# Kernel tuning notes

Measured on AMD Instinct MI355X. Metric: run time of the kernel, lower is better.

Reference implementation:

```python
import jax, jax.numpy as jnp
import numpy as np
from jax import lax

B, Hm, Wm = 8, 128, 128          # batch, mesh height, mesh width
DIM, HEADS, DH, G, K = 128, 8, 64, 64, 3
INNER = HEADS * DH
N = Hm * Wm


def setup_inputs() -> dict:
    key = jax.random.key(0)
    ks = jax.random.split(key, 12)
    s = 0.02
    x = jax.random.normal(ks[0], (B, N, DIM), dtype=jnp.float32)
    conv_fx_w = jax.random.normal(ks[1], (K, K, DIM, INNER), dtype=jnp.float32) * s
    conv_fx_b = jnp.zeros((INNER,), dtype=jnp.float32)
    conv_x_w = jax.random.normal(ks[2], (K, K, DIM, INNER), dtype=jnp.float32) * s
    conv_x_b = jnp.zeros((INNER,), dtype=jnp.float32)
    # nn.Linear(dim_head, slice_num): weight (G, DH), orthogonal-init approximated by scaled normal
    slice_w = jax.random.normal(ks[3], (G, DH), dtype=jnp.float32) * (1.0 / np.sqrt(DH))
    slice_b = jnp.zeros((G,), dtype=jnp.float32)
    temperature = jnp.ones((1, HEADS, 1, 1), dtype=jnp.float32) * 0.5
    wq = jax.random.normal(ks[4], (DH, DH), dtype=jnp.float32) * s
    wk = jax.random.normal(ks[5], (DH, DH), dtype=jnp.float32) * s
    wv = jax.random.normal(ks[6], (DH, DH), dtype=jnp.float32) * s
    out_w = jax.random.normal(ks[7], (DIM, INNER), dtype=jnp.float32) * s
    out_b = jnp.zeros((DIM,), dtype=jnp.float32)
    return {
        "x": x,
        "conv_fx_w": conv_fx_w, "conv_fx_b": conv_fx_b,
        "conv_x_w": conv_x_w, "conv_x_b": conv_x_b,
        "slice_w": slice_w, "slice_b": slice_b,
        "temperature": temperature,
        "wq": wq, "wk": wk, "wv": wv,
        "out_w": out_w, "out_b": out_b,
    }


def _conv(z, w, b):
    # z: (B, H, W, Cin); w: (K, K, Cin, Cout); SAME padding, stride 1
    return lax.conv_general_dilated(
        z, w, window_strides=(1, 1), padding="SAME",
        dimension_numbers=("NHWC", "HWIO", "NHWC")) + b


def reference(x, conv_fx_w, conv_fx_b, conv_x_w, conv_x_b,
              slice_w, slice_b, temperature, wq, wk, wv, out_w, out_b):
    b, n, c = x.shape
    xi = x.reshape(b, Hm, Wm, c)
    # (B,H,W,INNER) -> (B,N,heads,dh) -> (B,heads,N,dh)
    fx_mid = _conv(xi, conv_fx_w, conv_fx_b).reshape(b, n, HEADS, DH).transpose(0, 2, 1, 3)
    x_mid = _conv(xi, conv_x_w, conv_x_b).reshape(b, n, HEADS, DH).transpose(0, 2, 1, 3)

    temp = jnp.clip(temperature, 0.1, 5.0)  # (1,heads,1,1)
    logits = (jnp.einsum("bhnc,gc->bhng", x_mid, slice_w) + slice_b) / temp
    slice_weights = jax.nn.softmax(logits, axis=-1)         # (B,heads,N,G)

    slice_norm = slice_weights.sum(axis=2)                   # (B,heads,G)
    slice_token = jnp.einsum("bhnc,bhng->bhgc", fx_mid, slice_weights)
    slice_token = slice_token / (slice_norm + 1e-5)[..., None]

    q = jnp.einsum("bhgc,dc->bhgd", slice_token, wq)
    k = jnp.einsum("bhgc,dc->bhgd", slice_token, wk)
    v = jnp.einsum("bhgc,dc->bhgd", slice_token, wv)

    scale = DH ** (-0.5)
    attn = jax.nn.softmax(jnp.einsum("bhgd,bhkd->bhgk", q, k) * scale, axis=-1)
    out_slice = jnp.einsum("bhgk,bhkd->bhgd", attn, v)       # (B,heads,G,dh)

    out_x = jnp.einsum("bhgc,bhng->bhnc", out_slice, slice_weights)
    out_x = out_x.transpose(0, 2, 1, 3).reshape(b, n, INNER)
    return jnp.einsum("bnc,dc->bnd", out_x, out_w) + out_b
```

## Files before the change

### kernel.cpp

```cpp
#include <hip/hip_runtime.h>
#include <stdint.h>

#define BATCH 8
#define HEADS 8
#define HM 128
#define WM 128
#define NPIX (HM*WM)
#define DIMC 128
#define DH 64
#define GS 64
#define INNER 512
#define KTOT 1152
#define XT_LD 128
#define PT_LD 128

typedef unsigned short u16;
typedef short v8s __attribute__((ext_vector_type(8)));
typedef float v4f __attribute__((ext_vector_type(4)));

__device__ __forceinline__ u16 f2bf(float f) {
    unsigned x = __float_as_uint(f);
    return (u16)((x + 0x7fffu + ((x >> 16) & 1u)) >> 16);
}
__device__ __forceinline__ float bf2f(u16 u) { return __uint_as_float(((unsigned)u) << 16); }
__device__ __forceinline__ unsigned cvtpk(float lo, float hi) {
    unsigned r;
    asm("v_cvt_pk_bf16_f32 %0, %1, %2" : "=v"(r) : "v"(lo), "v"(hi));
    return r;
}

union BF8 { uint4 v; u16 s[8]; };

__global__ __launch_bounds__(256) void k_build_w(
    const float* __restrict__ wx, const float* __restrict__ wfx,
    const float* __restrict__ slw, const float* __restrict__ temp,
    u16* __restrict__ wcatT, u16* __restrict__ wfxT)
{
    __shared__ float sw_l[GS][DH + 1];
    __shared__ float wx_l[INNER];
    int row = blockIdx.x;
    int t = threadIdx.x;
    for (int i = t; i < GS * DH; i += 256) sw_l[i >> 6][i & 63] = slw[i];
    for (int i = t; i < INNER; i += 256) wx_l[i] = wx[(size_t)row * INNER + i];
    __syncthreads();
#pragma unroll
    for (int j = 0; j < 2; j++) {
        int co = j * 256 + t;
        int h = co >> 6, g = co & 63;
        float s = 0.f;
        for (int c = 0; c < DH; c++) s = fmaf(wx_l[h * 64 + c], sw_l[g][c], s);
        float tv = fminf(fmaxf(temp[h], 0.1f), 5.0f);
        wcatT[(size_t)co * KTOT + row] = f2bf(s / tv);
        wfxT[(size_t)co * KTOT + row] = f2bf(wfx[(size_t)row * INNER + co]);
    }
}

__global__ __launch_bounds__(512) void k_build_b(
    const float* __restrict__ bx, const float* __restrict__ slw,
    const float* __restrict__ slb, const float* __restrict__ temp,
    float* __restrict__ bcatL)
{
    int co = threadIdx.x;
    int h = co >> 6, g = co & 63;
    float s = slb[g];
    for (int c = 0; c < DH; c++) s = fmaf(bx[h * 64 + c], slw[g * 64 + c], s);
    float tv = fminf(fmaxf(temp[h], 0.1f), 5.0f);
    bcatL[co] = s / tv;
}

union SmemC {
    u16 X[130 * XT_LD];
    struct { u16 SwT[128][PT_LD]; u16 FxT[128][PT_LD]; } e;
};

__global__ __launch_bounds__(512) void k_conv2(
    const float* __restrict__ xin, const u16* __restrict__ wcatT,
    const u16* __restrict__ wfxT, const float* __restrict__ bcatL,
    const float* __restrict__ bfx, u16* __restrict__ swbT,
    float* __restrict__ straw, float* __restrict__ norm)
{
    __shared__ SmemC sm;
    int pt = blockIdx.x;
    int b = pt >> 7, y = pt & 127;
    int ct = blockIdx.y;
    int cob = ct << 8;
    int t = threadIdx.x;
    int lane = t & 63, wave = t >> 6;
    int w_half = wave >> 2, w_co = wave & 3;
    int l16 = lane & 15, lk = lane >> 4;
    int hb = b * HEADS + 4 * ct;

    v4f accL[4][4], accF[4][4];
#pragma unroll
    for (int i = 0; i < 4; i++)
#pragma unroll
        for (int j = 0; j < 4; j++) {
            accL[i][j] = v4f{0.f, 0.f, 0.f, 0.f};
            accF[i][j] = v4f{0.f, 0.f, 0.f, 0.f};
        }

    const u16* wlb[4]; const u16* wfb[4];
#pragma unroll
    for (int nj = 0; nj < 4; nj++) {
        size_t roff = (size_t)(cob + w_co * 64 + nj * 16 + l16) * KTOT + lk * 8;
        wlb[nj] = wcatT + roff;
        wfb[nj] = wfxT + roff;
    }

    v8s bL[2][4], bF[2][4];
#pragma unroll
    for (int nj = 0; nj < 4; nj++) {
        bL[0][nj] = *(const v8s*)(wlb[nj]);
        bF[0][nj] = *(const v8s*)(wfb[nj]);
    }

#pragma unroll
    for (int ky = 0; ky < 3; ky++) {
        int yy = y + ky - 1;
        bool yok = (unsigned)yy < (unsigned)HM;
        const float* xrow = xin + ((size_t)b * NPIX + (size_t)yy * WM) * DIMC;
        if (ky) __syncthreads();
#pragma unroll
        for (int it = 0; it < 5; it++) {
            int i = t + it * 512;
            if (i < 2080) {
                int row = i >> 4, k8 = i & 15;
                int px = row - 1;
                uint4 o;
                if (yok && (unsigned)px < (unsigned)WM) {
                    const float4* p = (const float4*)(xrow + (size_t)px * DIMC + k8 * 8);
                    float4 fa = p[0], fb = p[1];
                    o = make_uint4(cvtpk(fa.x, fa.y), cvtpk(fa.z, fa.w),
                                   cvtpk(fb.x, fb.y), cvtpk(fb.z, fb.w));
                } else {
                    o = make_uint4(0u, 0u, 0u, 0u);
                }
                *(uint4*)(sm.X + row * XT_LD + ((k8 ^ (row & 7)) * 8)) = o;
            }
        }
        __syncthreads();
#pragma unroll
        for (int cc = 0; cc < 12; cc++) {
            int g = ky * 12 + cc;
            if (g < 35) {
                int wo = ((g + 1) >> 2) * 128 + ((g + 1) & 3) * 32;
#pragma unroll
                for (int nj = 0; nj < 4; nj++) {
                    bL[(cc + 1) & 1][nj] = *(const v8s*)(wlb[nj] + wo);
                    bF[(cc + 1) & 1][nj] = *(const v8s*)(wfb[nj] + wo);
                }
            }
            int kx = cc >> 2, c4 = cc & 3;
            int xr7 = (l16 + kx) & 7;
            const u16* xb = sm.X + (w_half * 64 + l16 + kx) * XT_LD;
            int xo = (((c4 * 4 + lk) ^ xr7) * 8);
            v8s av[4];
#pragma unroll
            for (int mi = 0; mi < 4; mi++)
                av[mi] = *(const v8s*)(xb + mi * 16 * XT_LD + xo);
#pragma unroll
            for (int mi = 0; mi < 4; mi++)
#pragma unroll
                for (int nj = 0; nj < 4; nj++) {
                    accL[mi][nj] = __builtin_amdgcn_mfma_f32_16x16x32_bf16(
                        av[mi], bL[cc & 1][nj], accL[mi][nj], 0, 0, 0);
                    accF[mi][nj] = __builtin_amdgcn_mfma_f32_16x16x32_bf16(
                        av[mi], bF[cc & 1][nj], accF[mi][nj], 0, 0, 0);
                }
        }
    }
    __syncthreads();

    float bbL[4], bbF[4];
#pragma unroll
    for (int nj = 0; nj < 4; nj++) {
        bbL[nj] = bcatL[cob + w_co * 64 + nj * 16 + l16];
        bbF[nj] = bfx[cob + w_co * 64 + nj * 16 + l16];
    }

#pragma unroll
    for (int mi = 0; mi < 4; mi++) {
#pragma unroll
        for (int q = 0; q < 4; q++) {
            float m = accL[mi][0][q] + bbL[0];
#pragma unroll
            for (int nj = 1; nj < 4; nj++) m = fmaxf(m, accL[mi][nj][q] + bbL[nj]);
            m = fmaxf(m, __shfl_xor(m, 1));
            m = fmaxf(m, __shfl_xor(m, 2));
            m = fmaxf(m, __shfl_xor(m, 4));
            m = fmaxf(m, __shfl_xor(m, 8));
            float ssum = 0.f;
#pragma unroll
            for (int nj = 0; nj < 4; nj++) {
                float e = __expf(accL[mi][nj][q] + bbL[nj] - m);
                accL[mi][nj][q] = e; ssum += e;
            }
            ssum += __shfl_xor(ssum, 1);
            ssum += __shfl_xor(ssum, 2);
            ssum += __shfl_xor(ssum, 4);
            ssum += __shfl_xor(ssum, 8);
            float inv = 1.f / ssum;
#pragma unroll
            for (int nj = 0; nj < 4; nj++) accL[mi][nj][q] *= inv;
        }
    }

#pragma unroll
    for (int nj = 0; nj < 4; nj++) {
        float pn = 0.f;
#pragma unroll
        for (int mi = 0; mi < 4; mi++)
#pragma unroll
            for (int q = 0; q < 4; q++) pn += accL[mi][nj][q];
        pn += __shfl_xor(pn, 16);
        pn += __shfl_xor(pn, 32);
        if (lk == 0)
            atomicAdd(&norm[(size_t)(hb + w_co) * GS + nj * 16 + l16], pn);
    }

#pragma unroll
    for (int hp = 0; hp < 2; hp++) {
        bool mine = ((w_co >> 1) == hp);
        if (mine) {
            int wcp = w_co & 1;
#pragma unroll
            for (int nj = 0; nj < 4; nj++) {
                int grow = wcp * 64 + nj * 16 + l16;
                int r7 = l16 & 7;
#pragma unroll
                for (int mi = 0; mi < 4; mi++) {
                    int off = (((w_half * 8 + mi * 2 + (lk >> 1)) ^ r7) * 8) + (lk & 1) * 4;
                    uint2 wv;
                    wv.x = cvtpk(accL[mi][nj][0], accL[mi][nj][1]);
                    wv.y = cvtpk(accL[mi][nj][2], accL[mi][nj][3]);
                    *(uint2*)&sm.e.SwT[grow][off] = wv;
                    uint2 fv;
                    fv.x = cvtpk(accF[mi][nj][0] + bbF[nj], accF[mi][nj][1] + bbF[nj]);
                    fv.y = cvtpk(accF[mi][nj][2] + bbF[nj], accF[mi][nj][3] + bbF[nj]);
                    *(uint2*)&sm.e.FxT[grow][off] = fv;
                }
            }
        }
        __syncthreads();
        if (mine) {
            int wcp = w_co & 1;
            v4f pacc[2][4];
#pragma unroll
            for (int i = 0; i < 2; i++)
#pragma unroll
                for (int j = 0; j < 4; j++) pacc[i][j] = v4f{0.f, 0.f, 0.f, 0.f};
            int r7 = l16 & 7;
#pragma unroll
            for (int c = 0; c < 4; c++) {
                int ko = (((c * 4 + lk) ^ r7) * 8);
                v8s aw[2], bw[4];
#pragma unroll
                for (int mi = 0; mi < 2; mi++)
                    aw[mi] = *(const v8s*)(&sm.e.SwT[wcp * 64 + w_half * 32 + mi * 16 + l16][0] + ko);
#pragma unroll
                for (int nj = 0; nj < 4; nj++)
                    bw[nj] = *(const v8s*)(&sm.e.FxT[wcp * 64 + nj * 16 + l16][0] + ko);
#pragma unroll
                for (int mi = 0; mi < 2; mi++)
#pragma unroll
                    for (int nj = 0; nj < 4; nj++)
                        pacc[mi][nj] = __builtin_amdgcn_mfma_f32_16x16x32_bf16(
                            aw[mi], bw[nj], pacc[mi][nj], 0, 0, 0);
            }
            int bh2 = hb + 2 * hp + wcp;
#pragma unroll
            for (int mi = 0; mi < 2; mi++)
#pragma unroll
                for (int nj = 0; nj < 4; nj++)
#pragma unroll
                    for (int q = 0; q < 4; q++) {
                        int g = w_half * 32 + mi * 16 + lk * 4 + q;
                        int dh = nj * 16 + l16;
                        atomicAdd(&straw[((size_t)bh2 * GS + g) * DH + dh], pacc[mi][nj][q]);
                    }
        }
#pragma unroll
        for (int it = 0; it < 4; it++) {
            int chunk = it * 512 + t;
            int gi = chunk >> 4;
            int p8 = chunk & 15;
            uint4 v = *(const uint4*)(&sm.e.SwT[gi][0] + ((p8 ^ (gi & 7)) * 8));
            size_t di = (((size_t)(hb + 2 * hp + (gi >> 6)) * GS + (gi & 63)) * NPIX)
                        + (size_t)y * WM + p8 * 8;
            *(uint4*)&swbT[di] = v;
        }
        __syncthreads();
    }
}

__global__ __launch_bounds__(256) void k_attn(
    const float* __restrict__ straw, const float* __restrict__ norm,
    const float* __restrict__ wq, const float* __restrict__ wk, const float* __restrict__ wv,
    const float* __restrict__ outw, float* __restrict__ m1)
{
    __shared__ float lds[4][64][64];
    int bh = blockIdx.x, h = bh & 7;
    int t = threadIdx.x;
    for (int i = t; i < 4096; i += 256) {
        int g = i >> 6;
        lds[0][g][i & 63] = straw[(size_t)bh * 4096 + i] / (norm[bh * 64 + g] + 1e-5f);
    }
    __syncthreads();
    int g = t >> 2, d0 = (t & 3) << 4;
    for (int d = d0; d < d0 + 16; d++) {
        float sq = 0.f, sk = 0.f, sv = 0.f;
        for (int c = 0; c < 64; c++) {
            float sc = lds[0][g][c];
            sq = fmaf(sc, wq[d * 64 + c], sq);
            sk = fmaf(sc, wk[d * 64 + c], sk);
            sv = fmaf(sc, wv[d * 64 + c], sv);
        }
        lds[1][g][d] = sq; lds[2][g][d] = sk; lds[3][g][d] = sv;
    }
    __syncthreads();
    float attnrow[16];
    for (int k2 = d0, i = 0; k2 < d0 + 16; k2++, i++) {
        float s = 0.f;
        for (int d = 0; d < 64; d++) s = fmaf(lds[1][g][d], lds[2][k2][d], s);
        attnrow[i] = s * 0.125f;
    }
    __syncthreads();
    for (int i = 0; i < 16; i++) lds[0][g][d0 + i] = attnrow[i];
    __syncthreads();
    if (t < 64) {
        float mx = -1e30f;
        for (int j = 0; j < 64; j++) mx = fmaxf(mx, lds[0][t][j]);
        float s = 0.f;
        for (int j = 0; j < 64; j++) { float e = __expf(lds[0][t][j] - mx); lds[0][t][j] = e; s += e; }
        float inv = 1.f / s;
        for (int j = 0; j < 64; j++) lds[0][t][j] *= inv;
    }
    __syncthreads();
    float osrow[16];
    for (int d = d0, i = 0; d < d0 + 16; d++, i++) {
        float s = 0.f;
        for (int kx = 0; kx < 64; kx++) s = fmaf(lds[0][g][kx], lds[3][kx][d], s);
        osrow[i] = s;
    }
    __syncthreads();
    for (int i = 0; i < 16; i++) lds[2][g][d0 + i] = osrow[i];
    __syncthreads();
    int dimb = (t & 3) << 5;
    for (int dim = dimb; dim < dimb + 32; dim++) {
        float s = 0.f;
        for (int c = 0; c < 64; c++)
            s = fmaf(lds[2][g][c], outw[(size_t)dim * INNER + h * 64 + c], s);
        m1[((size_t)bh * 64 + g) * DIMC + dim] = s;
    }
}

__global__ __launch_bounds__(256) void k_final(
    const u16* __restrict__ swbT, const float* __restrict__ m1,
    const float* __restrict__ outb, float* __restrict__ out)
{
    __shared__ float As[32][68];
    __shared__ float Bs[32][128];
    int b = blockIdx.x, nt = blockIdx.y;
    int t = threadIdx.x;
    int tn = t & 15, tm = t >> 4;
    float acc[4][8];
#pragma unroll
    for (int i = 0; i < 4; i++)
#pragma unroll
        for (int j = 0; j < 8; j++) acc[i][j] = 0.f;
    int n0 = nt * 64;
    int gg = t >> 3, nq = (t & 7) * 8;
    int g2 = t >> 3, dd = (t & 7) * 16;
    for (int h = 0; h < HEADS; h++) {
        const u16* swp = swbT + (size_t)(b * HEADS + h) * GS * NPIX;
        const float* m1p = m1 + (size_t)(b * HEADS + h) * GS * DIMC;
        for (int g0 = 0; g0 < 64; g0 += 32) {
            __syncthreads();
            BF8 av8; av8.v = *(const uint4*)&swp[(size_t)(g0 + gg) * NPIX + n0 + nq];
#pragma unroll
            for (int i = 0; i < 8; i++) As[gg][nq + i] = bf2f(av8.s[i]);
            const float* bp = m1p + (size_t)(g0 + g2) * DIMC + dd;
            *(float4*)&Bs[g2][dd + 0]  = *(const float4*)(bp + 0);
            *(float4*)&Bs[g2][dd + 4]  = *(const float4*)(bp + 4);
            *(float4*)&Bs[g2][dd + 8]  = *(const float4*)(bp + 8);
            *(float4*)&Bs[g2][dd + 12] = *(const float4*)(bp + 12);
            __syncthreads();
#pragma unroll
            for (int kk = 0; kk < 32; kk++) {
                float4 a = *(const float4*)&As[kk][tm * 4];
                float4 b0 = *(const float4*)&Bs[kk][tn * 4];
                float4 b1 = *(const float4*)&Bs[kk][tn * 4 + 64];
                float av[4] = {a.x, a.y, a.z, a.w};
                float bv[8] = {b0.x, b0.y, b0.z, b0.w, b1.x, b1.y, b1.z, b1.w};
#pragma unroll
                for (int i = 0; i < 4; i++)
#pragma unroll
                    for (int j = 0; j < 8; j++)
                        acc[i][j] = fmaf(av[i], bv[j], acc[i][j]);
            }
        }
    }
    float4 bias0 = *(const float4*)&outb[tn * 4];
    float4 bias1 = *(const float4*)&outb[64 + tn * 4];
#pragma unroll
    for (int i = 0; i < 4; i++) {
        size_t n = (size_t)n0 + tm * 4 + i;
        size_t rb = ((size_t)b * NPIX + n) * DIMC;
        float4 r0, r1;
        r0.x = acc[i][0] + bias0.x; r0.y = acc[i][1] + bias0.y;
        r0.z = acc[i][2] + bias0.z; r0.w = acc[i][3] + bias0.w;
        r1.x = acc[i][4] + bias1.x; r1.y = acc[i][5] + bias1.y;
        r1.z = acc[i][6] + bias1.z; r1.w = acc[i][7] + bias1.w;
        *(float4*)&out[rb + tn * 4] = r0;
        *(float4*)&out[rb + 64 + tn * 4] = r1;
    }
}

extern "C" void kernel_launch(void* const* d_in, const int* in_sizes, int n_in,
                              void* d_out, int out_size, void* d_ws, size_t ws_size,
                              hipStream_t stream)
{
    (void)in_sizes; (void)n_in; (void)out_size;
    const float* x    = (const float*)d_in[0];
    const float* wfx  = (const float*)d_in[1];
    const float* bfx  = (const float*)d_in[2];
    const float* wx   = (const float*)d_in[3];
    const float* bx   = (const float*)d_in[4];
    const float* slw  = (const float*)d_in[5];
    const float* slb  = (const float*)d_in[6];
    const float* temp = (const float*)d_in[7];
    const float* wq   = (const float*)d_in[8];
    const float* wk   = (const float*)d_in[9];
    const float* wv   = (const float*)d_in[10];
    const float* outw = (const float*)d_in[11];
    const float* outb = (const float*)d_in[12];
    float* out = (float*)d_out;
    float* W = (float*)d_ws;

    u16*   wcatT = (u16*)W;
    u16*   wfxT  = (u16*)(W + 294912);
    float* bcatL = W + 589824;
    float* norm  = W + 590336;
    float* straw = W + 594432;
    float* m1    = W + 856576;
    u16*   swbT  = (u16*)(W + 1380864);
    const size_t need = 1380864ull * 4 + 67108864ull * 2;
    if (ws_size < need) return;

    hipMemsetAsync(norm, 0, (4096 + 262144) * sizeof(float), stream);

    k_build_w<<<dim3(1152), 256, 0, stream>>>(wx, wfx, slw, temp, wcatT, wfxT);
    k_build_b<<<dim3(1), 512, 0, stream>>>(bx, slw, slb, temp, bcatL);
    k_conv2<<<dim3(1024, 2), 512, 0, stream>>>(x, wcatT, wfxT, bcatL, bfx, swbT, straw, norm);
    k_attn<<<dim3(64), 256, 0, stream>>>(straw, norm, wq, wk, wv, outw, m1);
    k_final<<<dim3(8, 256), 256, 0, stream>>>(swbT, m1, outb, out);
}
```

Measured before the change: 1.192 ms.

## Shrink conv tiles to half-row, two heads per block, split conv paths across waves

Each conv block now handles a 64-pixel half row and 128 output channels (two heads) with 256 threads. Waves are split so that half compute the logit conv and half compute the fx conv, which halves accumulator registers per wave and allows 4 blocks per CU. The grid is swizzled so that consecutive blocks share inputs across channel tiles. The aim is higher occupancy and better latency hiding. In exchange, x loads are repeated more often across channel tiles, more blocks issue atomics into straw and norm, and the weight double-buffer prefetch is removed.

```diff
diff --git a/kernel.cpp b/kernel.cpp
--- a/kernel.cpp
+++ b/kernel.cpp
@@ -12,7 +12,6 @@
 #define INNER 512
 #define KTOT 1152
 #define XT_LD 128
-#define PT_LD 128
 
 typedef unsigned short u16;
 typedef short v8s __attribute__((ext_vector_type(8)));
@@ -69,50 +68,39 @@
 }
 
 union SmemC {
-    u16 X[130 * XT_LD];
-    struct { u16 SwT[128][PT_LD]; u16 FxT[128][PT_LD]; } e;
+    u16 X[66 * XT_LD];
+    struct { u16 SwT[64][64]; u16 FxT[64][64]; } e;
 };
 
-__global__ __launch_bounds__(512) void k_conv2(
+__global__ __launch_bounds__(256, 4) void k_conv2(
     const float* __restrict__ xin, const u16* __restrict__ wcatT,
     const u16* __restrict__ wfxT, const float* __restrict__ bcatL,
     const float* __restrict__ bfx, u16* __restrict__ swbT,
     float* __restrict__ straw, float* __restrict__ norm)
 {
     __shared__ SmemC sm;
-    int pt = blockIdx.x;
-    int b = pt >> 7, y = pt & 127;
-    int ct = blockIdx.y;
-    int cob = ct << 8;
+    int bid = blockIdx.x;
+    int swz = (bid & 7) * 1024 + (bid >> 3);
+    int b = swz >> 10;
+    int r = swz & 1023;
+    int y = r >> 3, half = (r >> 2) & 1, ct = r & 3;
+    int cob = ct << 7;
     int t = threadIdx.x;
     int lane = t & 63, wave = t >> 6;
-    int w_half = wave >> 2, w_co = wave & 3;
+    int w_conv = wave >> 1, w_co = wave & 1;
     int l16 = lane & 15, lk = lane >> 4;
-    int hb = b * HEADS + 4 * ct;
-
-    v4f accL[4][4], accF[4][4];
+
+    v4f acc[4][4];
 #pragma unroll
     for (int i = 0; i < 4; i++)
 #pragma unroll
-        for (int j = 0; j < 4; j++) {
-            accL[i][j] = v4f{0.f, 0.f, 0.f, 0.f};
-            accF[i][j] = v4f{0.f, 0.f, 0.f, 0.f};
-        }
-
-    const u16* wlb[4]; const u16* wfb[4];
-#pragma unroll
-    for (int nj = 0; nj < 4; nj++) {
-        size_t roff = (size_t)(cob + w_co * 64 + nj * 16 + l16) * KTOT + lk * 8;
-        wlb[nj] = wcatT + roff;
-        wfb[nj] = wfxT + roff;
-    }
-
-    v8s bL[2][4], bF[2][4];
-#pragma unroll
-    for (int nj = 0; nj < 4; nj++) {
-        bL[0][nj] = *(const v8s*)(wlb[nj]);
-        bF[0][nj] = *(const v8s*)(wfb[nj]);
-    }
+        for (int j = 0; j < 4; j++) acc[i][j] = v4f{0.f, 0.f, 0.f, 0.f};
+
+    const u16* wT = w_conv ? wfxT : wcatT;
+    const u16* wrb[4];
+#pragma unroll
+    for (int nj = 0; nj < 4; nj++)
+        wrb[nj] = wT + (size_t)(cob + w_co * 64 + nj * 16 + l16) * KTOT + lk * 8;
 
 #pragma unroll
     for (int ky = 0; ky < 3; ky++) {
@@ -122,10 +110,10 @@
         if (ky) __syncthreads();
 #pragma unroll
         for (int it = 0; it < 5; it++) {
-            int i = t + it * 512;
-            if (i < 2080) {
+            int i = t + it * 256;
+            if (i < 1056) {
                 int row = i >> 4, k8 = i & 15;
-                int px = row - 1;
+                int px = half * 64 + row - 1;
                 uint4 o;
                 if (yok && (unsigned)px < (unsigned)WM) {
                     const float4* p = (const float4*)(xrow + (size_t)px * DIMC + k8 * 8);
@@ -141,109 +129,101 @@
         __syncthreads();
 #pragma unroll
         for (int cc = 0; cc < 12; cc++) {
-            int g = ky * 12 + cc;
-            if (g < 35) {
-                int wo = ((g + 1) >> 2) * 128 + ((g + 1) & 3) * 32;
+            int kx = cc >> 2, c4 = cc & 3;
+            int wo = (ky * 3 + kx) * 128 + c4 * 32;
+            v8s bB[4];
+#pragma unroll
+            for (int nj = 0; nj < 4; nj++)
+                bB[nj] = *(const v8s*)(wrb[nj] + wo);
+            int xr7 = (l16 + kx) & 7;
+            const u16* xb = sm.X + (l16 + kx) * XT_LD;
+            int xo = (((c4 * 4 + lk) ^ xr7) * 8);
+            v8s av[4];
+#pragma unroll
+            for (int mi = 0; mi < 4; mi++)
+                av[mi] = *(const v8s*)(xb + mi * 16 * XT_LD + xo);
+#pragma unroll
+            for (int mi = 0; mi < 4; mi++)
+#pragma unroll
+                for (int nj = 0; nj < 4; nj++)
+                    acc[mi][nj] = __builtin_amdgcn_mfma_f32_16x16x32_bf16(
+                        av[mi], bB[nj], acc[mi][nj], 0, 0, 0);
+        }
+    }
+    __syncthreads();
+
+    float bb[4];
+#pragma unroll
+    for (int nj = 0; nj < 4; nj++)
+        bb[nj] = (w_conv ? bfx : bcatL)[cob + w_co * 64 + nj * 16 + l16];
+
+    if (w_conv == 0) {
+#pragma unroll
+        for (int mi = 0; mi < 4; mi++) {
+#pragma unroll
+            for (int q = 0; q < 4; q++) {
+                float m = acc[mi][0][q] + bb[0];
+#pragma unroll
+                for (int nj = 1; nj < 4; nj++) m = fmaxf(m, acc[mi][nj][q] + bb[nj]);
+                m = fmaxf(m, __shfl_xor(m, 1));
+                m = fmaxf(m, __shfl_xor(m, 2));
+                m = fmaxf(m, __shfl_xor(m, 4));
+                m = fmaxf(m, __shfl_xor(m, 8));
+                float ssum = 0.f;
 #pragma unroll
                 for (int nj = 0; nj < 4; nj++) {
-                    bL[(cc + 1) & 1][nj] = *(const v8s*)(wlb[nj] + wo);
-                    bF[(cc + 1) & 1][nj] = *(const v8s*)(wfb[nj] + wo);
+                    float e = __expf(acc[mi][nj][q] + bb[nj] - m);
+                    acc[mi][nj][q] = e; ssum += e;
+                }
+                ssum += __shfl_xor(ssum, 1);
+                ssum += __shfl_xor(ssum, 2);
+                ssum += __shfl_xor(ssum, 4);
+                ssum += __shfl_xor(ssum, 8);
+                float inv = 1.f / ssum;
+#pragma unroll
+                for (int nj = 0; nj < 4; nj++) acc[mi][nj][q] *= inv;
+            }
+        }
+#pragma unroll
+        for (int nj = 0; nj < 4; nj++) {
+            float pn = 0.f;
+#pragma unroll
+            for (int mi = 0; mi < 4; mi++)
+#pragma unroll
+                for (int q = 0; q < 4; q++) pn += acc[mi][nj][q];
+            pn += __shfl_xor(pn, 16);
+            pn += __shfl_xor(pn, 32);
+            if (lk == 0)
+                atomicAdd(&norm[(size_t)(b * HEADS + 2 * ct + w_co) * GS + nj * 16 + l16], pn);
+        }
+    }
+
+#pragma unroll
+    for (int hp = 0; hp < 2; hp++) {
+        bool mine = (w_co == hp);
+        if (mine) {
+#pragma unroll
+            for (int nj = 0; nj < 4; nj++) {
+                int grow = nj * 16 + l16;
+                int r7 = l16 & 7;
+#pragma unroll
+                for (int mi = 0; mi < 4; mi++) {
+                    int off = (((mi * 2 + (lk >> 1)) ^ r7) * 8) + (lk & 1) * 4;
+                    uint2 wv;
+                    if (w_conv == 0) {
+                        wv.x = cvtpk(acc[mi][nj][0], acc[mi][nj][1]);
+                        wv.y = cvtpk(acc[mi][nj][2], acc[mi][nj][3]);
+                        *(uint2*)&sm.e.SwT[grow][off] = wv;
+                    } else {
+                        wv.x = cvtpk(acc[mi][nj][0] + bb[nj], acc[mi][nj][1] + bb[nj]);
+                        wv.y = cvtpk(acc[mi][nj][2] + bb[nj], acc[mi][nj][3] + bb[nj]);
+                        *(uint2*)&sm.e.FxT[grow][off] = wv;
+                    }
                 }
             }
-            int kx = cc >> 2, c4 = cc & 3;
-            int xr7 = (l16 + kx) & 7;
-            const u16* xb = sm.X + (w_half * 64 + l16 + kx) * XT_LD;
-            int xo = (((c4 * 4 + lk) ^ xr7) * 8);
-            v8s av[4];
-#pragma unroll
-            for (int mi = 0; mi < 4; mi++)
-                av[mi] = *(const v8s*)(xb + mi * 16 * XT_LD + xo);
-#pragma unroll
-            for (int mi = 0; mi < 4; mi++)
-#pragma unroll
-                for (int nj = 0; nj < 4; nj++) {
-                    accL[mi][nj] = __builtin_amdgcn_mfma_f32_16x16x32_bf16(
-                        av[mi], bL[cc & 1][nj], accL[mi][nj], 0, 0, 0);
-                    accF[mi][nj] = __builtin_amdgcn_mfma_f32_16x16x32_bf16(
-                        av[mi], bF[cc & 1][nj], accF[mi][nj], 0, 0, 0);
-                }
-        }
-    }
-    __syncthreads();
-
-    float bbL[4], bbF[4];
-#pragma unroll
-    for (int nj = 0; nj < 4; nj++) {
-        bbL[nj] = bcatL[cob + w_co * 64 + nj * 16 + l16];
-        bbF[nj] = bfx[cob + w_co * 64 + nj * 16 + l16];
-    }
-
-#pragma unroll
-    for (int mi = 0; mi < 4; mi++) {
-#pragma unroll
-        for (int q = 0; q < 4; q++) {
-            float m = accL[mi][0][q] + bbL[0];
-#pragma unroll
-            for (int nj = 1; nj < 4; nj++) m = fmaxf(m, accL[mi][nj][q] + bbL[nj]);
-            m = fmaxf(m, __shfl_xor(m, 1));
-            m = fmaxf(m, __shfl_xor(m, 2));
-            m = fmaxf(m, __shfl_xor(m, 4));
-            m = fmaxf(m, __shfl_xor(m, 8));
-            float ssum = 0.f;
-#pragma unroll
-            for (int nj = 0; nj < 4; nj++) {
-                float e = __expf(accL[mi][nj][q] + bbL[nj] - m);
-                accL[mi][nj][q] = e; ssum += e;
-            }
-            ssum += __shfl_xor(ssum, 1);
-            ssum += __shfl_xor(ssum, 2);
-            ssum += __shfl_xor(ssum, 4);
-            ssum += __shfl_xor(ssum, 8);
-            float inv = 1.f / ssum;
-#pragma unroll
-            for (int nj = 0; nj < 4; nj++) accL[mi][nj][q] *= inv;
-        }
-    }
-
-#pragma unroll
-    for (int nj = 0; nj < 4; nj++) {
-        float pn = 0.f;
-#pragma unroll
-        for (int mi = 0; mi < 4; mi++)
-#pragma unroll
-            for (int q = 0; q < 4; q++) pn += accL[mi][nj][q];
-        pn += __shfl_xor(pn, 16);
-        pn += __shfl_xor(pn, 32);
-        if (lk == 0)
-            atomicAdd(&norm[(size_t)(hb + w_co) * GS + nj * 16 + l16], pn);
-    }
-
-#pragma unroll
-    for (int hp = 0; hp < 2; hp++) {
-        bool mine = ((w_co >> 1) == hp);
-        if (mine) {
-            int wcp = w_co & 1;
-#pragma unroll
-            for (int nj = 0; nj < 4; nj++) {
-                int grow = wcp * 64 + nj * 16 + l16;
-                int r7 = l16 & 7;
-#pragma unroll
-                for (int mi = 0; mi < 4; mi++) {
-                    int off = (((w_half * 8 + mi * 2 + (lk >> 1)) ^ r7) * 8) + (lk & 1) * 4;
-                    uint2 wv;
-                    wv.x = cvtpk(accL[mi][nj][0], accL[mi][nj][1]);
-                    wv.y = cvtpk(accL[mi][nj][2], accL[mi][nj][3]);
-                    *(uint2*)&sm.e.SwT[grow][off] = wv;
-                    uint2 fv;
-                    fv.x = cvtpk(accF[mi][nj][0] + bbF[nj], accF[mi][nj][1] + bbF[nj]);
-                    fv.y = cvtpk(accF[mi][nj][2] + bbF[nj], accF[mi][nj][3] + bbF[nj]);
-                    *(uint2*)&sm.e.FxT[grow][off] = fv;
-                }
-            }
         }
         __syncthreads();
         if (mine) {
-            int wcp = w_co & 1;
             v4f pacc[2][4];
 #pragma unroll
             for (int i = 0; i < 2; i++)
@@ -251,15 +231,15 @@
                 for (int j = 0; j < 4; j++) pacc[i][j] = v4f{0.f, 0.f, 0.f, 0.f};
             int r7 = l16 & 7;
 #pragma unroll
-            for (int c = 0; c < 4; c++) {
+            for (int c = 0; c < 2; c++) {
                 int ko = (((c * 4 + lk) ^ r7) * 8);
                 v8s aw[2], bw[4];
 #pragma unroll
                 for (int mi = 0; mi < 2; mi++)
-                    aw[mi] = *(const v8s*)(&sm.e.SwT[wcp * 64 + w_half * 32 + mi * 16 + l16][0] + ko);
+                    aw[mi] = *(const v8s*)(&sm.e.SwT[w_conv * 32 + mi * 16 + l16][0] + ko);
 #pragma unroll
                 for (int nj = 0; nj < 4; nj++)
-                    bw[nj] = *(const v8s*)(&sm.e.FxT[wcp * 64 + nj * 16 + l16][0] + ko);
+                    bw[nj] = *(const v8s*)(&sm.e.FxT[nj * 16 + l16][0] + ko);
 #pragma unroll
                 for (int mi = 0; mi < 2; mi++)
 #pragma unroll
@@ -267,26 +247,26 @@
                         pacc[mi][nj] = __builtin_amdgcn_mfma_f32_16x16x32_bf16(
                             aw[mi], bw[nj], pacc[mi][nj], 0, 0, 0);
             }
-            int bh2 = hb + 2 * hp + wcp;
+            int bh2 = b * HEADS + 2 * ct + hp;
 #pragma unroll
             for (int mi = 0; mi < 2; mi++)
 #pragma unroll
                 for (int nj = 0; nj < 4; nj++)
 #pragma unroll
                     for (int q = 0; q < 4; q++) {
-                        int g = w_half * 32 + mi * 16 + lk * 4 + q;
+                        int g = w_conv * 32 + mi * 16 + lk * 4 + q;
                         int dh = nj * 16 + l16;
                         atomicAdd(&straw[((size_t)bh2 * GS + g) * DH + dh], pacc[mi][nj][q]);
                     }
         }
 #pragma unroll
-        for (int it = 0; it < 4; it++) {
-            int chunk = it * 512 + t;
-            int gi = chunk >> 4;
-            int p8 = chunk & 15;
+        for (int it = 0; it < 2; it++) {
+            int chunk = it * 256 + t;
+            int gi = chunk >> 3;
+            int p8 = chunk & 7;
             uint4 v = *(const uint4*)(&sm.e.SwT[gi][0] + ((p8 ^ (gi & 7)) * 8));
-            size_t di = (((size_t)(hb + 2 * hp + (gi >> 6)) * GS + (gi & 63)) * NPIX)
-                        + (size_t)y * WM + p8 * 8;
+            size_t di = (((size_t)(b * HEADS + 2 * ct + hp) * GS + gi) * NPIX)
+                        + (size_t)y * WM + half * 64 + p8 * 8;
             *(uint4*)&swbT[di] = v;
         }
         __syncthreads();
@@ -451,7 +431,7 @@
 
     k_build_w<<<dim3(1152), 256, 0, stream>>>(wx, wfx, slw, temp, wcatT, wfxT);
     k_build_b<<<dim3(1), 512, 0, stream>>>(bx, slw, slb, temp, bcatL);
-    k_conv2<<<dim3(1024, 2), 512, 0, stream>>>(x, wcatT, wfxT, bcatL, bfx, swbT, straw, norm);
+    k_conv2<<<dim3(8192), 256, 0, stream>>>(x, wcatT, wfxT, bcatL, bfx, swbT, straw, norm);
     k_attn<<<dim3(64), 256, 0, stream>>>(straw, norm, wq, wk, wv, outw, m1);
     k_final<<<dim3(8, 256), 256, 0, stream>>>(swbT, m1, outb, out);
 }
```

Result: slower. 1.228 ms (+3.1%).
